# Optimization experiments

Hardware: AMD Instinct MI355X
Metric: run time of the kernel (lower is better)

Reference implementation:

```python
import jax, jax.numpy as jnp
import numpy as np

N = 50000      # nodes
E = 800000     # edges
F_IN = 128     # n_features
H = 4          # n_heads
C1 = 64        # n_hidden (per-head out of layer 1)
C2 = 32        # n_classes (per-head out of layer 2)
NEG_SLOPE = 0.2
EPS = 1e-16


def setup_inputs() -> dict:
    key = jax.random.key(0)
    ks = jax.random.split(key, 12)
    x = jax.random.normal(ks[0], (N, F_IN), dtype=jnp.float32)
    edge_index = jax.random.randint(ks[1], (2, E), 0, N, dtype=jnp.int64)
    # layer 1 params (GATConv: shared lin for src/dst, att_src/att_dst vectors, bias)
    W1 = jax.random.normal(ks[2], (F_IN, H * C1), dtype=jnp.float32) * (1.0 / np.sqrt(F_IN))
    att_src1 = jax.random.normal(ks[3], (H, C1), dtype=jnp.float32) * 0.1
    att_dst1 = jax.random.normal(ks[4], (H, C1), dtype=jnp.float32) * 0.1
    b1 = jnp.zeros((C1,), dtype=jnp.float32)
    # layer 2 params
    W2 = jax.random.normal(ks[5], (C1, H * C2), dtype=jnp.float32) * (1.0 / np.sqrt(C1))
    att_src2 = jax.random.normal(ks[6], (H, C2), dtype=jnp.float32) * 0.1
    att_dst2 = jax.random.normal(ks[7], (H, C2), dtype=jnp.float32) * 0.1
    b2 = jnp.zeros((C2,), dtype=jnp.float32)
    return {"x": x, "edge_index": edge_index,
            "W1": W1, "att_src1": att_src1, "att_dst1": att_dst1, "b1": b1,
            "W2": W2, "att_src2": att_src2, "att_dst2": att_dst2, "b2": b2}


def gat_conv(x, src, dst, W, att_src, att_dst, b, heads, out_ch):
    """PyG GATConv with concat=False (head-averaged output)."""
    n = x.shape[0]
    h = (x @ W).reshape(n, heads, out_ch)                 # [N, H, C]
    a_s = jnp.einsum('nhc,hc->nh', h, att_src)            # [N, H]
    a_d = jnp.einsum('nhc,hc->nh', h, att_dst)            # [N, H]
    e = jax.nn.leaky_relu(a_s[src] + a_d[dst], NEG_SLOPE)  # [E, H]
    # segment softmax over edges grouped by destination node
    m = jax.ops.segment_max(e, dst, num_segments=n)        # [N, H]
    m = jnp.where(jnp.isfinite(m), m, 0.0)
    ex = jnp.exp(e - m[dst])                               # [E, H]
    denom = jax.ops.segment_sum(ex, dst, num_segments=n)   # [N, H]
    alpha = ex / (denom[dst] + EPS)                        # [E, H]
    # scatter-add aggregation of attended source features
    msg = alpha[:, :, None] * h[src]                       # [E, H, C]
    out = jax.ops.segment_sum(msg, dst, num_segments=n)    # [N, H, C]
    return out.mean(axis=1) + b                            # [N, C]


def reference(x, edge_index, W1, att_src1, att_dst1, b1, W2, att_src2, att_dst2, b2):
    src, dst = edge_index[0], edge_index[1]
    h = jax.nn.relu(gat_conv(x, src, dst, W1, att_src1, att_dst1, b1, H, C1))
    # dropout is identity in eval mode
    out = gat_conv(h, src, dst, W2, att_src2, att_dst2, b2, H, C2)
    return out
```

## Files before the change

### kernel.cpp

```cpp
#include <hip/hip_runtime.h>
#include <hip/hip_fp16.h>
#include <cstdint>
#include <cstddef>

#define N_NODES 50000
#define N_EDGES 800000
#define F_IN 128
#define H_HEADS 4
#define C1 64
#define C2 32
#define NEG_SLOPE 0.2f
#define EPS_GAT 1e-16f
#define SLOT_CAP 96
#define FILL_BPG 256
#define NODES_PER_GROUP 6250
#define CBASE ((int)0xAAAAAAAAu)

typedef _Float16 half8 __attribute__((ext_vector_type(8)));
typedef float f32x4 __attribute__((ext_vector_type(4)));

template<int K, int M>
__device__ __forceinline__ void wtrans_dev(const float* __restrict__ W,
                                           _Float16* __restrict__ Wt,
                                           _Float16* tile, int bm, int bk) {
    const int m0 = bm * 64, k0 = bk * 64;
    const int t = threadIdx.x;
    const int c = t & 63;
#pragma unroll
    for (int j = 0; j < 16; ++j) {
        int r = (t >> 6) + 4 * j;
        tile[c * 66 + r] = (_Float16)W[(size_t)(k0 + r) * M + m0 + c];
    }
    __syncthreads();
#pragma unroll
    for (int j = 0; j < 16; ++j) {
        int m_l = (t >> 6) + 4 * j;
        Wt[(size_t)(m0 + m_l) * K + k0 + c] = tile[m_l * 66 + c];
    }
}

__global__ __launch_bounds__(256) void fill_wtrans_kernel(
        const int* __restrict__ src, const int* __restrict__ dst,
        int* __restrict__ cursor, unsigned short* __restrict__ slots,
        const float* __restrict__ W1, _Float16* __restrict__ wt1,
        const float* __restrict__ W2, _Float16* __restrict__ wt2) {
    __shared__ _Float16 tile[64 * 66];
    const int b = blockIdx.x;
    if (b < 8) {
        wtrans_dev<F_IN, H_HEADS * C1>(W1, wt1, tile, b & 3, b >> 2);
    } else if (b < 10) {
        wtrans_dev<C1, H_HEADS * C2>(W2, wt2, tile, b - 8, 0);
    }
    const int g = b & 7;
    const int bg = b >> 3;
    const int dlo = g * NODES_PER_GROUP;
    const int dhi = dlo + NODES_PER_GROUP;
    const int4* dst4 = (const int4*)dst;
    const int4* src4 = (const int4*)src;
    constexpr int NV4 = N_EDGES / 4;
    for (int v = bg * 256 + (int)threadIdx.x; v < NV4; v += FILL_BPG * 256) {
        int4 d4 = dst4[v];
        int4 s4 = src4[v];
        if (d4.x >= dlo && d4.x < dhi) {
            unsigned int p = (unsigned int)(atomicAdd(&cursor[d4.x], 1) - CBASE);
            if (p < SLOT_CAP) slots[(size_t)d4.x * SLOT_CAP + p] = (unsigned short)s4.x;
        }
        if (d4.y >= dlo && d4.y < dhi) {
            unsigned int p = (unsigned int)(atomicAdd(&cursor[d4.y], 1) - CBASE);
            if (p < SLOT_CAP) slots[(size_t)d4.y * SLOT_CAP + p] = (unsigned short)s4.y;
        }
        if (d4.z >= dlo && d4.z < dhi) {
            unsigned int p = (unsigned int)(atomicAdd(&cursor[d4.z], 1) - CBASE);
            if (p < SLOT_CAP) slots[(size_t)d4.z * SLOT_CAP + p] = (unsigned short)s4.z;
        }
        if (d4.w >= dlo && d4.w < dhi) {
            unsigned int p = (unsigned int)(atomicAdd(&cursor[d4.w], 1) - CBASE);
            if (p < SLOT_CAP) slots[(size_t)d4.w * SLOT_CAP + p] = (unsigned short)s4.w;
        }
    }
}

template<int K, int M, int Hn, int C, typename InT>
__global__ __launch_bounds__(256) void gemm_att_kernel(
        const InT* __restrict__ X, const _Float16* __restrict__ Wt,
        _Float16* __restrict__ Hout,
        const float* __restrict__ atts, const float* __restrict__ attd,
        float* __restrict__ as_, float* __restrict__ ad_, int Nr) {
    constexpr int LDK = K + 8;
    constexpr int NCT = M / 64;
    constexpr int HPB = 64 / C;
    __shared__ _Float16 Ah[64 * LDK];
    __shared__ _Float16 Bt[64 * LDK];
    __shared__ _Float16 Ht[64 * 72];
    const int row0 = blockIdx.x * 64;
    const int t = threadIdx.x;
    const int wv = t >> 6;
    const int lane = t & 63;
    const int quad = lane >> 4;
    const int n16 = lane & 15;

    if constexpr (sizeof(InT) == 4) {
        constexpr int KQ = K / 4;
#pragma unroll
        for (int j = 0; j < (64 * KQ) / 256; ++j) {
            int flat = t + 256 * j;
            int r = flat / KQ, kq = flat % KQ;
            int rg = row0 + r;
            float4 v = make_float4(0.f, 0.f, 0.f, 0.f);
            if (rg < Nr) v = *(const float4*)&X[(size_t)rg * K + 4 * kq];
            _Float16 tmp[4] = {(_Float16)v.x, (_Float16)v.y, (_Float16)v.z, (_Float16)v.w};
            *(uint2*)&Ah[r * LDK + 4 * kq] = *(const uint2*)tmp;
        }
    } else {
        constexpr int KQ = K / 8;
#pragma unroll
        for (int j = 0; j < (64 * KQ) / 256; ++j) {
            int flat = t + 256 * j;
            int r = flat / KQ, kq = flat % KQ;
            int rg = row0 + r;
            uint4 v = make_uint4(0u, 0u, 0u, 0u);
            if (rg < Nr) v = *(const uint4*)&X[(size_t)rg * K + 8 * kq];
            *(uint4*)&Ah[r * LDK + 8 * kq] = v;
        }
    }
    __syncthreads();

    half8 af[K / 32];
    const _Float16* Ap = &Ah[(16 * wv + n16) * LDK + 8 * quad];
#pragma unroll
    for (int ki = 0; ki < K / 32; ++ki) af[ki] = *(const half8*)(Ap + 32 * ki);

    for (int ct = 0; ct < NCT; ++ct) {
        const int col0 = 64 * ct;
        __syncthreads();
        {
            constexpr int KQ8 = K / 8;
#pragma unroll
            for (int j = 0; j < (64 * KQ8) / 256; ++j) {
                int flat = t + 256 * j;
                int c = flat / KQ8, kq = flat % KQ8;
                uint4 v = *(const uint4*)&Wt[(size_t)(col0 + c) * K + 8 * kq];
                *(uint4*)&Bt[c * LDK + 8 * kq] = v;
            }
        }
        __syncthreads();

        f32x4 acc[4];
#pragma unroll
        for (int nf = 0; nf < 4; ++nf) acc[nf] = (f32x4){0.f, 0.f, 0.f, 0.f};
#pragma unroll
        for (int ki = 0; ki < K / 32; ++ki) {
#pragma unroll
            for (int nf = 0; nf < 4; ++nf) {
                half8 bf = *(const half8*)&Bt[(16 * nf + n16) * LDK + 32 * ki + 8 * quad];
                acc[nf] = __builtin_amdgcn_mfma_f32_16x16x32_f16(af[ki], bf, acc[nf], 0, 0, 0);
            }
        }

        float dps[HPB][4], dpd[HPB][4];
#pragma unroll
        for (int u = 0; u < HPB; ++u)
#pragma unroll
            for (int r = 0; r < 4; ++r) { dps[u][r] = 0.f; dpd[u][r] = 0.f; }
#pragma unroll
        for (int nf = 0; nf < 4; ++nf) {
            int gc = col0 + 16 * nf + n16;
            float cs = atts[gc], cd = attd[gc];
#pragma unroll
            for (int r = 0; r < 4; ++r) {
                float av = acc[nf][r];
                dps[(16 * nf) / C][r] += av * cs;
                dpd[(16 * nf) / C][r] += av * cd;
            }
        }
#pragma unroll
        for (int u = 0; u < HPB; ++u)
#pragma unroll
            for (int r = 0; r < 4; ++r) {
                float s = dps[u][r], d = dpd[u][r];
#pragma unroll
                for (int off = 1; off < 16; off <<= 1) {
                    s += __shfl_xor(s, off, 64);
                    d += __shfl_xor(d, off, 64);
                }
                dps[u][r] = s; dpd[u][r] = d;
            }
        if (n16 == 0) {
            const int h0 = col0 / C;
#pragma unroll
            for (int r = 0; r < 4; ++r) {
                int row = row0 + 16 * wv + 4 * quad + r;
                if (row < Nr) {
#pragma unroll
                    for (int u = 0; u < HPB; ++u) {
                        as_[row * Hn + h0 + u] = dps[u][r];
                        ad_[row * Hn + h0 + u] = dpd[u][r];
                    }
                }
            }
        }

#pragma unroll
        for (int nf = 0; nf < 4; ++nf)
#pragma unroll
            for (int r = 0; r < 4; ++r)
                Ht[(16 * wv + 4 * quad + r) * 72 + 16 * nf + n16] = (_Float16)acc[nf][r];
        __syncthreads();
#pragma unroll
        for (int j = 0; j < 2; ++j) {
            int chunk = t + 256 * j;
            int r = chunk >> 3, cc = chunk & 7;
            int row = row0 + r;
            if (row < Nr) {
                uint4 v = *(const uint4*)&Ht[r * 72 + 8 * cc];
                *(uint4*)&Hout[(size_t)row * M + col0 + 8 * cc] = v;
            }
        }
    }
}

template<int Hn, int C, bool RELU, bool OUT_F16>
__global__ __launch_bounds__(256) void gat_agg_kernel(
        const int* __restrict__ degp, const unsigned short* __restrict__ slots,
        const float* __restrict__ as_, const float* __restrict__ ad_,
        const _Float16* __restrict__ Hm, const float* __restrict__ bias,
        void* __restrict__ outv, int Nr) {
    constexpr int HC = Hn * C;
    constexpr int PER = HC / 16;
    constexpr int NV = PER / 8;
    int node = blockIdx.x * 4 + (threadIdx.x >> 6);
    int lane = threadIdx.x & 63;
    if (node >= Nr) return;
    const int g = lane >> 4;
    const int l = lane & 15;
    const int h = l >> 2;
    const float ad_h = ad_[node * Hn + h];

    const int dn = min(degp[node] - CBASE, SLOT_CAP);
    const int begin = node * SLOT_CAP;
    const int end = begin + dn;
    const int iters = (dn + 3) >> 2;

    float acc[PER];
#pragma unroll
    for (int t = 0; t < PER; ++t) acc[t] = 0.f;
    float wsum = 0.f;

    int idx = begin + g;
    int s_cur = (idx < end) ? (int)slots[idx] : -1;
    int s_nx = (idx + 4 < end) ? (int)slots[idx + 4] : -1;
    float a_cur = 0.f;
    uint4 u_cur[NV] = {};
    if (s_cur >= 0) {
        a_cur = as_[s_cur * Hn + h];
        const uint4* hp = (const uint4*)(Hm + (size_t)s_cur * HC + l * PER);
        u_cur[0] = hp[0];
        if constexpr (NV == 2) u_cur[1] = hp[1];
    }

    for (int it = 0; it < iters; ++it) {
        const int s_pf = s_nx;
        s_nx = (idx + 8 < end) ? (int)slots[idx + 8] : -1;
        float a_nx = 0.f;
        uint4 u_nx[NV] = {};
        if (s_pf >= 0) {
            a_nx = as_[s_pf * Hn + h];
            const uint4* hp = (const uint4*)(Hm + (size_t)s_pf * HC + l * PER);
            u_nx[0] = hp[0];
            if constexpr (NV == 2) u_nx[1] = hp[1];
        }
        float logit = a_cur + ad_h;
        logit = (logit > 0.f) ? logit : NEG_SLOPE * logit;
        float w = (s_cur >= 0) ? __expf(logit) : 0.f;
        wsum += w;
#pragma unroll
        for (int v = 0; v < NV; ++v) {
            float2 f;
            f = __half22float2(*(const __half2*)&u_cur[v].x);
            acc[8 * v + 0] += w * f.x; acc[8 * v + 1] += w * f.y;
            f = __half22float2(*(const __half2*)&u_cur[v].y);
            acc[8 * v + 2] += w * f.x; acc[8 * v + 3] += w * f.y;
            f = __half22float2(*(const __half2*)&u_cur[v].z);
            acc[8 * v + 4] += w * f.x; acc[8 * v + 5] += w * f.y;
            f = __half22float2(*(const __half2*)&u_cur[v].w);
            acc[8 * v + 6] += w * f.x; acc[8 * v + 7] += w * f.y;
        }
        s_cur = s_pf; a_cur = a_nx;
#pragma unroll
        for (int v = 0; v < NV; ++v) u_cur[v] = u_nx[v];
        idx += 4;
    }

#pragma unroll
    for (int t = 0; t < PER; ++t) {
        acc[t] += __shfl_xor(acc[t], 16, 64);
        acc[t] += __shfl_xor(acc[t], 32, 64);
    }
    wsum += __shfl_xor(wsum, 16, 64);
    wsum += __shfl_xor(wsum, 32, 64);
    const float inv = 1.f / (wsum + EPS_GAT);
    float val[PER];
#pragma unroll
    for (int t = 0; t < PER; ++t) {
        float v = acc[t] * inv;
        v += __shfl_xor(v, 4, 64);
        v += __shfl_xor(v, 8, 64);
        val[t] = v * (1.0f / Hn);
    }
    if (lane < 4) {
        const int c0 = lane * PER;
#pragma unroll
        for (int t = 0; t < PER; ++t) {
            float v = val[t] + bias[c0 + t];
            if (RELU) v = fmaxf(v, 0.f);
            val[t] = v;
        }
        if constexpr (OUT_F16) {
            _Float16* o = (_Float16*)outv;
            _Float16 tmp[PER];
#pragma unroll
            for (int t = 0; t < PER; ++t) tmp[t] = (_Float16)val[t];
            uint4* d4 = (uint4*)&o[(size_t)node * C + c0];
            d4[0] = *(const uint4*)&tmp[0];
            if constexpr (NV == 2) d4[1] = *(const uint4*)&tmp[8];
        } else {
            float* o = (float*)outv;
#pragma unroll
            for (int t4 = 0; t4 < PER / 4; ++t4)
                *(float4*)&o[(size_t)node * C + c0 + 4 * t4] =
                    make_float4(val[4 * t4 + 0], val[4 * t4 + 1],
                                val[4 * t4 + 2], val[4 * t4 + 3]);
        }
    }
}

extern "C" void kernel_launch(void* const* d_in, const int* in_sizes, int n_in,
                              void* d_out, int out_size, void* d_ws, size_t ws_size,
                              hipStream_t stream) {
    const float* x    = (const float*)d_in[0];
    const int*   ei   = (const int*)d_in[1];
    const float* W1   = (const float*)d_in[2];
    const float* as1w = (const float*)d_in[3];
    const float* ad1w = (const float*)d_in[4];
    const float* b1   = (const float*)d_in[5];
    const float* W2   = (const float*)d_in[6];
    const float* as2w = (const float*)d_in[7];
    const float* ad2w = (const float*)d_in[8];
    const float* b2   = (const float*)d_in[9];
    float* out = (float*)d_out;

    const int* src = ei;
    const int* dst = ei + N_EDGES;

    char* ws = (char*)d_ws;
    size_t off = 0;
    auto alloc = [&](size_t bytes) -> void* {
        void* p = ws + off;
        off = (off + bytes + 255) & ~(size_t)255;
        return p;
    };
    int*   cursor = (int*)alloc((size_t)N_NODES * 4);
    float* as1_ = (float*)alloc((size_t)N_NODES * H_HEADS * 4);
    float* ad1_ = (float*)alloc((size_t)N_NODES * H_HEADS * 4);
    float* as2_ = (float*)alloc((size_t)N_NODES * H_HEADS * 4);
    float* ad2_ = (float*)alloc((size_t)N_NODES * H_HEADS * 4);
    _Float16* h1   = (_Float16*)alloc((size_t)N_NODES * H_HEADS * C1 * 2);
    _Float16* out1 = (_Float16*)alloc((size_t)N_NODES * C1 * 2);
    _Float16* h2   = (_Float16*)alloc((size_t)N_NODES * H_HEADS * C2 * 2);
    _Float16* wt1  = (_Float16*)alloc((size_t)(H_HEADS * C1) * F_IN * 2);
    _Float16* wt2  = (_Float16*)alloc((size_t)(H_HEADS * C2) * C1 * 2);
    unsigned short* slots = (unsigned short*)alloc((size_t)N_NODES * SLOT_CAP * 2);

    fill_wtrans_kernel<<<8 * FILL_BPG, 256, 0, stream>>>(
        src, dst, cursor, slots, W1, wt1, W2, wt2);

    gemm_att_kernel<F_IN, H_HEADS * C1, H_HEADS, C1, float>
        <<<(N_NODES + 63) / 64, 256, 0, stream>>>(
            x, wt1, h1, as1w, ad1w, as1_, ad1_, N_NODES);

    gat_agg_kernel<H_HEADS, C1, true, true><<<(N_NODES + 3) / 4, 256, 0, stream>>>(
        cursor, slots, as1_, ad1_, h1, b1, (void*)out1, N_NODES);

    gemm_att_kernel<C1, H_HEADS * C2, H_HEADS, C2, _Float16>
        <<<(N_NODES + 63) / 64, 256, 0, stream>>>(
            out1, wt2, h2, as2w, ad2w, as2_, ad2_, N_NODES);

    gat_agg_kernel<H_HEADS, C2, false, false><<<(N_NODES + 3) / 4, 256, 0, stream>>>(
        cursor, slots, as2_, ad2_, h2, b2, (void*)out, N_NODES);
}
```

Before: 250.4 us.

## Fuse layer-1 aggregation with layer-2 GEMM and attention projections

Replaces the separate layer-1 aggregation kernel and layer-2 GEMM kernel with one kernel. Each 64-node block aggregates its nodes into shared memory, then runs MFMA against the transposed W2 to produce h2 and the attention logits. This drops the out1 round trip through global memory and one kernel launch. In exchange, blocks go from 4 to 64 nodes each and each wave walks 16 nodes one after another, which lowers parallelism and latency hiding during the gather. The aggregation also skips the per-node max subtraction in the softmax exp.

```diff
diff --git a/kernel.cpp b/kernel.cpp
--- a/kernel.cpp
+++ b/kernel.cpp
@@ -219,6 +219,177 @@
     }
 }
 
+__global__ __launch_bounds__(256) void agg1_gemm2_kernel(
+        const int* __restrict__ degp, const unsigned short* __restrict__ slots,
+        const float* __restrict__ as_, const float* __restrict__ ad_,
+        const _Float16* __restrict__ Hm, const float* __restrict__ bias,
+        const _Float16* __restrict__ wt2,
+        const float* __restrict__ atts2, const float* __restrict__ attd2,
+        float* __restrict__ as2o, float* __restrict__ ad2o,
+        _Float16* __restrict__ h2o, int Nr) {
+    constexpr int HC = H_HEADS * C1;
+    constexpr int PER = HC / 16;
+    __shared__ _Float16 Bt[128 * 72];
+    __shared__ _Float16 Ht[64 * 72];
+    const int node0 = blockIdx.x * 64;
+    const int t = threadIdx.x;
+    const int wv = t >> 6;
+    const int lane = t & 63;
+    const int quad = lane >> 4;
+    const int n16 = lane & 15;
+    const int g = lane >> 4;
+    const int l = lane & 15;
+    const int h = l >> 2;
+
+#pragma unroll
+    for (int j = 0; j < 4; ++j) {
+        int flat = t + 256 * j;
+        int c = flat >> 3, kq = flat & 7;
+        uint4 v = *(const uint4*)&wt2[(size_t)c * C1 + 8 * kq];
+        *(uint4*)&Bt[c * 72 + 8 * kq] = v;
+    }
+    __syncthreads();
+
+    for (int i = 0; i < 16; ++i) {
+        const int node = node0 + 16 * wv + i;
+        const int dn = (node < Nr) ? min(degp[node] - CBASE, SLOT_CAP) : 0;
+        const int begin = node * SLOT_CAP;
+        const int end = begin + dn;
+        const int iters = (dn + 3) >> 2;
+        const float ad_h = (node < Nr) ? ad_[node * H_HEADS + h] : 0.f;
+
+        float acc[PER];
+#pragma unroll
+        for (int tt = 0; tt < PER; ++tt) acc[tt] = 0.f;
+        float wsum = 0.f;
+
+        int idx = begin + g;
+        int s_cur = (idx < end) ? (int)slots[idx] : -1;
+        int s_nx = (idx + 4 < end) ? (int)slots[idx + 4] : -1;
+        float a_cur = 0.f;
+        uint4 u_cur[2] = {};
+        if (s_cur >= 0) {
+            a_cur = as_[s_cur * H_HEADS + h];
+            const uint4* hp = (const uint4*)(Hm + (size_t)s_cur * HC + l * PER);
+            u_cur[0] = hp[0]; u_cur[1] = hp[1];
+        }
+        for (int it = 0; it < iters; ++it) {
+            const int s_pf = s_nx;
+            s_nx = (idx + 8 < end) ? (int)slots[idx + 8] : -1;
+            float a_nx = 0.f;
+            uint4 u_nx[2] = {};
+            if (s_pf >= 0) {
+                a_nx = as_[s_pf * H_HEADS + h];
+                const uint4* hp = (const uint4*)(Hm + (size_t)s_pf * HC + l * PER);
+                u_nx[0] = hp[0]; u_nx[1] = hp[1];
+            }
+            float logit = a_cur + ad_h;
+            logit = (logit > 0.f) ? logit : NEG_SLOPE * logit;
+            float w = (s_cur >= 0) ? __expf(logit) : 0.f;
+            wsum += w;
+#pragma unroll
+            for (int v = 0; v < 2; ++v) {
+                float2 f;
+                f = __half22float2(*(const __half2*)&u_cur[v].x);
+                acc[8 * v + 0] += w * f.x; acc[8 * v + 1] += w * f.y;
+                f = __half22float2(*(const __half2*)&u_cur[v].y);
+                acc[8 * v + 2] += w * f.x; acc[8 * v + 3] += w * f.y;
+                f = __half22float2(*(const __half2*)&u_cur[v].z);
+                acc[8 * v + 4] += w * f.x; acc[8 * v + 5] += w * f.y;
+                f = __half22float2(*(const __half2*)&u_cur[v].w);
+                acc[8 * v + 6] += w * f.x; acc[8 * v + 7] += w * f.y;
+            }
+            s_cur = s_pf; a_cur = a_nx;
+            u_cur[0] = u_nx[0]; u_cur[1] = u_nx[1];
+            idx += 4;
+        }
+
+#pragma unroll
+        for (int tt = 0; tt < PER; ++tt) {
+            acc[tt] += __shfl_xor(acc[tt], 16, 64);
+            acc[tt] += __shfl_xor(acc[tt], 32, 64);
+        }
+        wsum += __shfl_xor(wsum, 16, 64);
+        wsum += __shfl_xor(wsum, 32, 64);
+        const float inv = 1.f / (wsum + EPS_GAT);
+        float val[PER];
+#pragma unroll
+        for (int tt = 0; tt < PER; ++tt) {
+            float v = acc[tt] * inv;
+            v += __shfl_xor(v, 4, 64);
+            v += __shfl_xor(v, 8, 64);
+            val[tt] = v * (1.0f / H_HEADS);
+        }
+        if (lane < 4) {
+            const int c0 = lane * PER;
+            _Float16 tmp[PER];
+#pragma unroll
+            for (int tt = 0; tt < PER; ++tt) {
+                float v = val[tt] + bias[c0 + tt];
+                tmp[tt] = (_Float16)fmaxf(v, 0.f);
+            }
+            uint4* d4 = (uint4*)&Ht[(16 * wv + i) * 72 + c0];
+            d4[0] = *(const uint4*)&tmp[0];
+            d4[1] = *(const uint4*)&tmp[8];
+        }
+    }
+
+    half8 af[2];
+    const _Float16* Ap = &Ht[(16 * wv + n16) * 72 + 8 * quad];
+#pragma unroll
+    for (int ki = 0; ki < 2; ++ki) af[ki] = *(const half8*)(Ap + 32 * ki);
+
+#pragma unroll
+    for (int hh = 0; hh < 4; ++hh) {
+        float dps[4] = {0.f, 0.f, 0.f, 0.f};
+        float dpd[4] = {0.f, 0.f, 0.f, 0.f};
+#pragma unroll
+        for (int sub = 0; sub < 2; ++sub) {
+            const int col0 = 32 * hh + 16 * sub;
+            f32x4 acc = (f32x4){0.f, 0.f, 0.f, 0.f};
+#pragma unroll
+            for (int ki = 0; ki < 2; ++ki) {
+                half8 bf = *(const half8*)&Bt[(col0 + n16) * 72 + 32 * ki + 8 * quad];
+                acc = __builtin_amdgcn_mfma_f32_16x16x32_f16(af[ki], bf, acc, 0, 0, 0);
+            }
+            float cs = atts2[col0 + n16], cd = attd2[col0 + n16];
+#pragma unroll
+            for (int r = 0; r < 4; ++r) {
+                dps[r] += acc[r] * cs;
+                dpd[r] += acc[r] * cd;
+            }
+#pragma unroll
+            for (int r = 0; r < 4; ++r)
+                Ht[(16 * wv + 4 * quad + r) * 72 + n16] = (_Float16)acc[r];
+            {
+                int rl = lane >> 2;
+                int ck = lane & 3;
+                int row = node0 + 16 * wv + rl;
+                if (row < Nr) {
+                    uint2 v = *(const uint2*)&Ht[(16 * wv + rl) * 72 + 4 * ck];
+                    *(uint2*)&h2o[(size_t)row * 128 + col0 + 4 * ck] = v;
+                }
+            }
+        }
+#pragma unroll
+        for (int r = 0; r < 4; ++r) {
+            float s = dps[r], d = dpd[r];
+#pragma unroll
+            for (int off = 1; off < 16; off <<= 1) {
+                s += __shfl_xor(s, off, 64);
+                d += __shfl_xor(d, off, 64);
+            }
+            if (n16 == 0) {
+                int row = node0 + 16 * wv + 4 * quad + r;
+                if (row < Nr) {
+                    as2o[row * H_HEADS + hh] = s;
+                    ad2o[row * H_HEADS + hh] = d;
+                }
+            }
+        }
+    }
+}
+
 template<int Hn, int C, bool RELU, bool OUT_F16>
 __global__ __launch_bounds__(256) void gat_agg_kernel(
         const int* __restrict__ degp, const unsigned short* __restrict__ slots,
@@ -365,7 +536,6 @@
     float* as2_ = (float*)alloc((size_t)N_NODES * H_HEADS * 4);
     float* ad2_ = (float*)alloc((size_t)N_NODES * H_HEADS * 4);
     _Float16* h1   = (_Float16*)alloc((size_t)N_NODES * H_HEADS * C1 * 2);
-    _Float16* out1 = (_Float16*)alloc((size_t)N_NODES * C1 * 2);
     _Float16* h2   = (_Float16*)alloc((size_t)N_NODES * H_HEADS * C2 * 2);
     _Float16* wt1  = (_Float16*)alloc((size_t)(H_HEADS * C1) * F_IN * 2);
     _Float16* wt2  = (_Float16*)alloc((size_t)(H_HEADS * C2) * C1 * 2);
@@ -378,12 +548,8 @@
         <<<(N_NODES + 63) / 64, 256, 0, stream>>>(
             x, wt1, h1, as1w, ad1w, as1_, ad1_, N_NODES);
 
-    gat_agg_kernel<H_HEADS, C1, true, true><<<(N_NODES + 3) / 4, 256, 0, stream>>>(
-        cursor, slots, as1_, ad1_, h1, b1, (void*)out1, N_NODES);
-
-    gemm_att_kernel<C1, H_HEADS * C2, H_HEADS, C2, _Float16>
-        <<<(N_NODES + 63) / 64, 256, 0, stream>>>(
-            out1, wt2, h2, as2w, ad2w, as2_, ad2_, N_NODES);
+    agg1_gemm2_kernel<<<(N_NODES + 63) / 64, 256, 0, stream>>>(
+        cursor, slots, as1_, ad1_, h1, b1, wt2, as2w, ad2w, as2_, ad2_, h2, N_NODES);
 
     gat_agg_kernel<H_HEADS, C2, false, false><<<(N_NODES + 3) / 4, 256, 0, stream>>>(
         cursor, slots, as2_, ad2_, h2, b2, (void*)out, N_NODES);
```

Result: slower. 267.5 us (+6.8%).
